# Kernel optimization log

Measured on AMD Instinct MI355X. Metric: run time of the kernel, lower is better.

## Reference

```python
import jax, jax.numpy as jnp
import numpy as np

B = 256        # graphs in batch
N_PER = 512    # nodes per graph (uniform)
D = 256        # in_dim
DEG = 16       # avg degree
RATIO = 0.5


def setup_inputs() -> dict:
    key = jax.random.key(0)
    k1, k2, k3, k4 = jax.random.split(key, 4)
    N = B * N_PER
    e_per = N_PER * DEG
    x = jax.random.normal(k1, (N, D), dtype=jnp.float32)
    # edges confined within each graph (DGL batched-graph structure)
    src = jax.random.randint(k2, (B, e_per), 0, N_PER)
    dst = jax.random.randint(k3, (B, e_per), 0, N_PER)
    offs = jnp.arange(B, dtype=jnp.int32)[:, None] * N_PER
    src = (src + offs).reshape(-1).astype(jnp.int32)
    dst = (dst + offs).reshape(-1).astype(jnp.int32)
    W = jax.random.normal(k4, (D, 1), dtype=jnp.float32) / np.sqrt(D)
    b = jnp.zeros((1,), dtype=jnp.float32)
    num_nodes = jnp.full((B,), N_PER, dtype=jnp.int32)
    return {"x": x, "W": W, "b": b, "src": src, "dst": dst, "num_nodes": num_nodes}


def reference(x, W, b, src, dst, num_nodes):
    N, d = x.shape
    bsz = num_nodes.shape[0]
    n = N // bsz                     # uniform nodes per graph -> static
    k = int(np.ceil(RATIO * n))      # nodes kept per graph (static)

    # ---- GraphConv(in_dim, 1), DGL default norm='both':
    # score = D_in^{-1/2} A D_out^{-1/2} (x W) + b   (W applied first: out_dim < in_dim)
    ones_e = jnp.ones(src.shape, dtype=x.dtype)
    deg_out = jax.ops.segment_sum(ones_e, src, num_segments=N)
    deg_in = jax.ops.segment_sum(ones_e, dst, num_segments=N)
    h = x @ W                                              # [N, 1]
    h = h * jax.lax.rsqrt(jnp.clip(deg_out, 1.0))[:, None]
    agg = jax.ops.segment_sum(h[src], dst, num_segments=N) # [N, 1]
    score = (agg * jax.lax.rsqrt(jnp.clip(deg_in, 1.0))[:, None] + b)[:, 0]  # [N]

    # ---- topk per graph: dense [B, n] buffer is just a reshape (uniform graphs),
    # sort descending + take first k  ==  lax.top_k
    dense = score.reshape(bsz, n)
    _, idx = jax.lax.top_k(dense, k)                       # [B, k] descending
    perm = (idx + jnp.arange(bsz)[:, None] * n).reshape(-1)  # global node ids [B*k]

    # ---- gather + scale: feature[perm] * tanh(score[perm])
    feat = x[perm] * jnp.tanh(score[perm])[:, None]        # [B*k, D]

    # ---- node_subgraph: edges whose both endpoints survive
    keep = jnp.zeros((N,), dtype=bool).at[perm].set(True)
    edge_mask = keep[src] & keep[dst]                      # [E]
    next_num_nodes = jnp.full((bsz,), k, dtype=jnp.int32)
    return feat, perm, edge_mask, next_num_nodes
```

## Files before the change

### kernel.cpp

```cpp
#include <hip/hip_runtime.h>
#include <math.h>

#define BB    256
#define NPER  512
#define DD    256
#define KK    256
#define EPG   (NPER * 16)
#define NN    (BB * NPER)
#define EE    (BB * EPG)

__global__ __launch_bounds__(256) void k_dot(const float* __restrict__ x,
                                             const float* __restrict__ W,
                                             float* __restrict__ hraw) {
    const int wave = threadIdx.x >> 6;
    const int lane = threadIdx.x & 63;
    const int r0   = blockIdx.x * 16 + wave * 4;
    const float4 wv = ((const float4*)W)[lane];
    const float4* p = (const float4*)(x + ((size_t)r0 << 8));
    float4 a0 = p[lane];
    float4 a1 = p[64 + lane];
    float4 a2 = p[128 + lane];
    float4 a3 = p[192 + lane];
    float d0 = a0.x * wv.x + a0.y * wv.y + a0.z * wv.z + a0.w * wv.w;
    float d1 = a1.x * wv.x + a1.y * wv.y + a1.z * wv.z + a1.w * wv.w;
    float d2 = a2.x * wv.x + a2.y * wv.y + a2.z * wv.z + a2.w * wv.w;
    float d3 = a3.x * wv.x + a3.y * wv.y + a3.z * wv.z + a3.w * wv.w;
    #pragma unroll
    for (int off = 32; off > 0; off >>= 1) {
        d0 += __shfl_down(d0, off, 64);
        d1 += __shfl_down(d1, off, 64);
        d2 += __shfl_down(d2, off, 64);
        d3 += __shfl_down(d3, off, 64);
    }
    if (lane == 0) {
        hraw[r0]     = d0;
        hraw[r0 + 1] = d1;
        hraw[r0 + 2] = d2;
        hraw[r0 + 3] = d3;
    }
}

__global__ __launch_bounds__(512) void k_graph(
        const float* __restrict__ hraw, const float* __restrict__ b,
        const int* __restrict__ src, const int* __restrict__ dst,
        int* __restrict__ perm_i, float* __restrict__ tscore,
        int* __restrict__ keepg, float* __restrict__ out_perm) {
    __shared__ unsigned short esrc[EPG];
    __shared__ unsigned short edst[EPG];
    __shared__ int   degs[NPER];
    __shared__ int   degd[NPER];
    __shared__ float hl[NPER];
    __shared__ float aggl[NPER];
    __shared__ float scl[NPER];
    __shared__ unsigned long long keys[NPER];
    __shared__ int   keep[NPER];

    const int g = blockIdx.x;
    const int t = threadIdx.x;
    const int nbase = g << 9;

    degs[t] = 0; degd[t] = 0; aggl[t] = 0.0f; keep[t] = 0;
    __syncthreads();

    const int4* s4 = (const int4*)(src + (size_t)g * EPG);
    const int4* d4 = (const int4*)(dst + (size_t)g * EPG);
    for (int i = t; i < EPG / 4; i += 512) {
        int4 sv = s4[i], dv = d4[i];
        int e = i * 4;
        unsigned short s0 = (unsigned short)(sv.x - nbase);
        unsigned short s1 = (unsigned short)(sv.y - nbase);
        unsigned short s2 = (unsigned short)(sv.z - nbase);
        unsigned short s3 = (unsigned short)(sv.w - nbase);
        esrc[e] = s0; esrc[e + 1] = s1; esrc[e + 2] = s2; esrc[e + 3] = s3;
        atomicAdd(&degs[s0], 1); atomicAdd(&degs[s1], 1);
        atomicAdd(&degs[s2], 1); atomicAdd(&degs[s3], 1);
        unsigned short t0 = (unsigned short)(dv.x - nbase);
        unsigned short t1 = (unsigned short)(dv.y - nbase);
        unsigned short t2 = (unsigned short)(dv.z - nbase);
        unsigned short t3 = (unsigned short)(dv.w - nbase);
        edst[e] = t0; edst[e + 1] = t1; edst[e + 2] = t2; edst[e + 3] = t3;
        atomicAdd(&degd[t0], 1); atomicAdd(&degd[t1], 1);
        atomicAdd(&degd[t2], 1); atomicAdd(&degd[t3], 1);
    }
    __syncthreads();

    hl[t] = hraw[nbase + t] * rsqrtf(fmaxf((float)degs[t], 1.0f));
    __syncthreads();

    for (int e = t; e < EPG; e += 512)
        atomicAdd(&aggl[edst[e]], hl[esrc[e]]);
    __syncthreads();

    scl[t] = aggl[t] * rsqrtf(fmaxf((float)degd[t], 1.0f)) + b[0];
    __syncthreads();

    {
        unsigned int u = __float_as_uint(scl[t]);
        u = (u & 0x80000000u) ? ~u : (u | 0x80000000u);
        keys[t] = ((unsigned long long)u << 32) |
                  (unsigned long long)(0xFFFFFFFFu - (unsigned)t);
    }
    __syncthreads();
    for (int kk = 2; kk <= NPER; kk <<= 1) {
        for (int j = kk >> 1; j > 0; j >>= 1) {
            int i = t, ixj = t ^ j;
            if (ixj > i) {
                unsigned long long a = keys[i], c = keys[ixj];
                bool up = ((i & kk) == 0);
                if (up ? (a < c) : (a > c)) { keys[i] = c; keys[ixj] = a; }
            }
            __syncthreads();
        }
    }
    if (t < KK) {
        unsigned long long kv = keys[t];
        int idx = (int)(0xFFFFFFFFu - (unsigned int)(kv & 0xFFFFFFFFull));
        int r = (g << 8) + t;
        perm_i[r]   = nbase + idx;
        out_perm[r] = (float)(nbase + idx);
        tscore[r]   = tanhf(scl[idx]);
        keep[idx]   = 1;
    }
    __syncthreads();
    keepg[nbase + t] = keep[t];
}

#define FEATBLK (BB * KK / 4)
#define MASKBLK (EE / 4 / 256)
__global__ __launch_bounds__(256) void k_featmask(
        const float* __restrict__ x,
        const int* __restrict__ perm_i, const float* __restrict__ tscore,
        const int* __restrict__ src, const int* __restrict__ dst,
        const int* __restrict__ keepg,
        float* __restrict__ feat, float* __restrict__ emask,
        float* __restrict__ nnn) {
    if (blockIdx.x < FEATBLK) {
        const int wave = threadIdx.x >> 6;
        const int lane = threadIdx.x & 63;
        const int r = blockIdx.x * 4 + wave;
        const int gid = perm_i[r];
        const float ts = tscore[r];
        float4 v = ((const float4*)(x + ((size_t)gid << 8)))[lane];
        float4 o = make_float4(v.x * ts, v.y * ts, v.z * ts, v.w * ts);
        ((float4*)(feat + ((size_t)r << 8)))[lane] = o;
    } else {
        const int mb = blockIdx.x - FEATBLK;
        const int i = mb * 256 + threadIdx.x;
        int4 sv = ((const int4*)src)[i];
        int4 dv = ((const int4*)dst)[i];
        float4 m;
        m.x = (keepg[sv.x] & keepg[dv.x]) ? 1.0f : 0.0f;
        m.y = (keepg[sv.y] & keepg[dv.y]) ? 1.0f : 0.0f;
        m.z = (keepg[sv.z] & keepg[dv.z]) ? 1.0f : 0.0f;
        m.w = (keepg[sv.w] & keepg[dv.w]) ? 1.0f : 0.0f;
        ((float4*)emask)[i] = m;
        if (mb == 0 && threadIdx.x < BB) nnn[threadIdx.x] = (float)KK;
    }
}

extern "C" void kernel_launch(void* const* d_in, const int* in_sizes, int n_in,
                              void* d_out, int out_size, void* d_ws, size_t ws_size,
                              hipStream_t stream) {
    const float* x   = (const float*)d_in[0];
    const float* W   = (const float*)d_in[1];
    const float* b   = (const float*)d_in[2];
    const int*   src = (const int*)d_in[3];
    const int*   dst = (const int*)d_in[4];

    float* out   = (float*)d_out;
    float* feat  = out;
    float* operm = feat + (size_t)BB * KK * DD;
    float* emask = operm + (size_t)BB * KK;
    float* nnn   = emask + (size_t)EE;

    float* hraw   = (float*)d_ws;
    int*   perm_i = (int*)(hraw + NN);
    float* tscore = (float*)(perm_i + BB * KK);
    int*   keepg  = (int*)(tscore + BB * KK);

    k_dot     <<<NN / 16, 256, 0, stream>>>(x, W, hraw);
    k_graph   <<<BB, 512, 0, stream>>>(hraw, b, src, dst, perm_i, tscore, keepg, operm);
    k_featmask<<<FEATBLK + MASKBLK, 256, 0, stream>>>(x, perm_i, tscore, src, dst,
                                                      keepg, feat, emask, nnn);
}
```

Measured before the change: 261.7 us.

## Fuse edge-mask computation into per-graph kernel using shared-memory edge lists

Edge-mask generation moves into the per-graph kernel, reusing the 16-bit local edge indices and keep flags already held in shared memory. This removes the global keep array and the second full read of src/dst in the last kernel. The graph kernel now runs with 1024 threads, packs edge index stores into 32-bit writes, and prefetches hraw early. In exchange, the mask work is confined to only 256 blocks, and the bitonic sort leaves half the threads idle while they still pay for the barriers.

```diff
diff --git a/kernel.cpp b/kernel.cpp
--- a/kernel.cpp
+++ b/kernel.cpp
@@ -40,11 +40,12 @@
     }
 }
 
-__global__ __launch_bounds__(512) void k_graph(
+__global__ __launch_bounds__(1024) void k_graph(
         const float* __restrict__ hraw, const float* __restrict__ b,
         const int* __restrict__ src, const int* __restrict__ dst,
         int* __restrict__ perm_i, float* __restrict__ tscore,
-        int* __restrict__ keepg, float* __restrict__ out_perm) {
+        float* __restrict__ out_perm, float* __restrict__ emask,
+        float* __restrict__ nnn) {
     __shared__ unsigned short esrc[EPG];
     __shared__ unsigned short edst[EPG];
     __shared__ int   degs[NPER];
@@ -59,59 +60,70 @@
     const int t = threadIdx.x;
     const int nbase = g << 9;
 
-    degs[t] = 0; degd[t] = 0; aggl[t] = 0.0f; keep[t] = 0;
+    float hv = 0.0f;
+    if (t < NPER) hv = hraw[nbase + t];
+
+    if (t < NPER) { degs[t] = 0; degd[t] = 0; aggl[t] = 0.0f; keep[t] = 0; }
     __syncthreads();
 
     const int4* s4 = (const int4*)(src + (size_t)g * EPG);
     const int4* d4 = (const int4*)(dst + (size_t)g * EPG);
-    for (int i = t; i < EPG / 4; i += 512) {
+    unsigned int* es2 = (unsigned int*)esrc;
+    unsigned int* ed2 = (unsigned int*)edst;
+    #pragma unroll
+    for (int i = t; i < EPG / 4; i += 1024) {
         int4 sv = s4[i], dv = d4[i];
-        int e = i * 4;
-        unsigned short s0 = (unsigned short)(sv.x - nbase);
-        unsigned short s1 = (unsigned short)(sv.y - nbase);
-        unsigned short s2 = (unsigned short)(sv.z - nbase);
-        unsigned short s3 = (unsigned short)(sv.w - nbase);
-        esrc[e] = s0; esrc[e + 1] = s1; esrc[e + 2] = s2; esrc[e + 3] = s3;
+        unsigned int s0 = (unsigned int)(sv.x - nbase);
+        unsigned int s1 = (unsigned int)(sv.y - nbase);
+        unsigned int s2 = (unsigned int)(sv.z - nbase);
+        unsigned int s3 = (unsigned int)(sv.w - nbase);
+        es2[i * 2]     = s0 | (s1 << 16);
+        es2[i * 2 + 1] = s2 | (s3 << 16);
         atomicAdd(&degs[s0], 1); atomicAdd(&degs[s1], 1);
         atomicAdd(&degs[s2], 1); atomicAdd(&degs[s3], 1);
-        unsigned short t0 = (unsigned short)(dv.x - nbase);
-        unsigned short t1 = (unsigned short)(dv.y - nbase);
-        unsigned short t2 = (unsigned short)(dv.z - nbase);
-        unsigned short t3 = (unsigned short)(dv.w - nbase);
-        edst[e] = t0; edst[e + 1] = t1; edst[e + 2] = t2; edst[e + 3] = t3;
+        unsigned int t0 = (unsigned int)(dv.x - nbase);
+        unsigned int t1 = (unsigned int)(dv.y - nbase);
+        unsigned int t2 = (unsigned int)(dv.z - nbase);
+        unsigned int t3 = (unsigned int)(dv.w - nbase);
+        ed2[i * 2]     = t0 | (t1 << 16);
+        ed2[i * 2 + 1] = t2 | (t3 << 16);
         atomicAdd(&degd[t0], 1); atomicAdd(&degd[t1], 1);
         atomicAdd(&degd[t2], 1); atomicAdd(&degd[t3], 1);
     }
     __syncthreads();
 
-    hl[t] = hraw[nbase + t] * rsqrtf(fmaxf((float)degs[t], 1.0f));
+    if (t < NPER) hl[t] = hv * rsqrtf(fmaxf((float)degs[t], 1.0f));
     __syncthreads();
 
-    for (int e = t; e < EPG; e += 512)
+    #pragma unroll
+    for (int e = t; e < EPG; e += 1024)
         atomicAdd(&aggl[edst[e]], hl[esrc[e]]);
     __syncthreads();
 
-    scl[t] = aggl[t] * rsqrtf(fmaxf((float)degd[t], 1.0f)) + b[0];
-    __syncthreads();
-
-    {
-        unsigned int u = __float_as_uint(scl[t]);
+    if (t < NPER) {
+        float sc = aggl[t] * rsqrtf(fmaxf((float)degd[t], 1.0f)) + b[0];
+        scl[t] = sc;
+        unsigned int u = __float_as_uint(sc);
         u = (u & 0x80000000u) ? ~u : (u | 0x80000000u);
         keys[t] = ((unsigned long long)u << 32) |
                   (unsigned long long)(0xFFFFFFFFu - (unsigned)t);
     }
     __syncthreads();
+
     for (int kk = 2; kk <= NPER; kk <<= 1) {
         for (int j = kk >> 1; j > 0; j >>= 1) {
-            int i = t, ixj = t ^ j;
-            if (ixj > i) {
-                unsigned long long a = keys[i], c = keys[ixj];
-                bool up = ((i & kk) == 0);
-                if (up ? (a < c) : (a > c)) { keys[i] = c; keys[ixj] = a; }
+            if (t < NPER) {
+                int i = t, ixj = t ^ j;
+                if (ixj > i) {
+                    unsigned long long a = keys[i], c = keys[ixj];
+                    bool up = ((i & kk) == 0);
+                    if (up ? (a < c) : (a > c)) { keys[i] = c; keys[ixj] = a; }
+                }
             }
             __syncthreads();
         }
     }
+
     if (t < KK) {
         unsigned long long kv = keys[t];
         int idx = (int)(0xFFFFFFFFu - (unsigned int)(kv & 0xFFFFFFFFull));
@@ -122,40 +134,33 @@
         keep[idx]   = 1;
     }
     __syncthreads();
-    keepg[nbase + t] = keep[t];
+
+    float4* em4 = (float4*)(emask + ((size_t)g << 13));
+    #pragma unroll
+    for (int i = t; i < EPG / 4; i += 1024) {
+        int e = i * 4;
+        float4 m;
+        m.x = (keep[esrc[e]]     & keep[edst[e]])     ? 1.0f : 0.0f;
+        m.y = (keep[esrc[e + 1]] & keep[edst[e + 1]]) ? 1.0f : 0.0f;
+        m.z = (keep[esrc[e + 2]] & keep[edst[e + 2]]) ? 1.0f : 0.0f;
+        m.w = (keep[esrc[e + 3]] & keep[edst[e + 3]]) ? 1.0f : 0.0f;
+        em4[i] = m;
+    }
+    if (g == 0 && t < BB) nnn[t] = (float)KK;
 }
 
-#define FEATBLK (BB * KK / 4)
-#define MASKBLK (EE / 4 / 256)
-__global__ __launch_bounds__(256) void k_featmask(
+__global__ __launch_bounds__(256) void k_feat(
         const float* __restrict__ x,
         const int* __restrict__ perm_i, const float* __restrict__ tscore,
-        const int* __restrict__ src, const int* __restrict__ dst,
-        const int* __restrict__ keepg,
-        float* __restrict__ feat, float* __restrict__ emask,
-        float* __restrict__ nnn) {
-    if (blockIdx.x < FEATBLK) {
-        const int wave = threadIdx.x >> 6;
-        const int lane = threadIdx.x & 63;
-        const int r = blockIdx.x * 4 + wave;
-        const int gid = perm_i[r];
-        const float ts = tscore[r];
-        float4 v = ((const float4*)(x + ((size_t)gid << 8)))[lane];
-        float4 o = make_float4(v.x * ts, v.y * ts, v.z * ts, v.w * ts);
-        ((float4*)(feat + ((size_t)r << 8)))[lane] = o;
-    } else {
-        const int mb = blockIdx.x - FEATBLK;
-        const int i = mb * 256 + threadIdx.x;
-        int4 sv = ((const int4*)src)[i];
-        int4 dv = ((const int4*)dst)[i];
-        float4 m;
-        m.x = (keepg[sv.x] & keepg[dv.x]) ? 1.0f : 0.0f;
-        m.y = (keepg[sv.y] & keepg[dv.y]) ? 1.0f : 0.0f;
-        m.z = (keepg[sv.z] & keepg[dv.z]) ? 1.0f : 0.0f;
-        m.w = (keepg[sv.w] & keepg[dv.w]) ? 1.0f : 0.0f;
-        ((float4*)emask)[i] = m;
-        if (mb == 0 && threadIdx.x < BB) nnn[threadIdx.x] = (float)KK;
-    }
+        float* __restrict__ feat) {
+    const int wave = threadIdx.x >> 6;
+    const int lane = threadIdx.x & 63;
+    const int r = blockIdx.x * 4 + wave;
+    const int gid = perm_i[r];
+    const float ts = tscore[r];
+    float4 v = ((const float4*)(x + ((size_t)gid << 8)))[lane];
+    float4 o = make_float4(v.x * ts, v.y * ts, v.z * ts, v.w * ts);
+    ((float4*)(feat + ((size_t)r << 8)))[lane] = o;
 }
 
 extern "C" void kernel_launch(void* const* d_in, const int* in_sizes, int n_in,
@@ -176,10 +181,9 @@
     float* hraw   = (float*)d_ws;
     int*   perm_i = (int*)(hraw + NN);
     float* tscore = (float*)(perm_i + BB * KK);
-    int*   keepg  = (int*)(tscore + BB * KK);
 
-    k_dot     <<<NN / 16, 256, 0, stream>>>(x, W, hraw);
-    k_graph   <<<BB, 512, 0, stream>>>(hraw, b, src, dst, perm_i, tscore, keepg, operm);
-    k_featmask<<<FEATBLK + MASKBLK, 256, 0, stream>>>(x, perm_i, tscore, src, dst,
-                                                      keepg, feat, emask, nnn);
+    k_dot  <<<NN / 16, 256, 0, stream>>>(x, W, hraw);
+    k_graph<<<BB, 1024, 0, stream>>>(hraw, b, src, dst, perm_i, tscore,
+                                     operm, emask, nnn);
+    k_feat <<<BB * KK / 4, 256, 0, stream>>>(x, perm_i, tscore, feat);
 }
```

After: 257.6 us. About the same (-1.6%).
